# Performance work log

Hardware: AMD Instinct MI355X
Metric: run time of the kernel (lower is better)

The kernel has to match this reference:

```python
import jax, jax.numpy as jnp
import numpy as np

G_OFF = 1e-4
G_ON = 1e-3
K_V = 0.25
B, N_IN, N_OUT = 512, 512, 512


def setup_inputs() -> dict:
    key = jax.random.key(0)
    k1, k2 = jax.random.split(key)
    x = jax.random.normal(k1, (B, N_IN), dtype=jnp.float32)
    # build(): w ~ N(0, 1/sqrt(neurons_in)), b = zeros
    w = jax.random.normal(k2, (N_IN, N_OUT), dtype=jnp.float32) * (1.0 / np.sqrt(N_IN))
    b = jnp.zeros((N_OUT,), dtype=jnp.float32)
    return {"x": x, "w": w, "b": b}


def reference(x, w, b):
    # forward(): append ones column to inputs, bias row to weights
    inputs = jnp.concatenate([x, jnp.ones((x.shape[0], 1), dtype=x.dtype)], axis=1)  # [B, in+1]
    weights = jnp.concatenate([w, b[None, :]], axis=0)                               # [in+1, out]

    voltages = K_V * inputs

    # mapping.weights_to_conductances, rule='lowest':
    # differential pair per weight, interleaved (even=pos, odd=neg)
    max_weight = jnp.max(jnp.abs(weights))
    k_cond = (G_ON - G_OFF) / max_weight
    g_eff = k_cond * weights
    g_pos = G_OFF + jnp.maximum(g_eff, 0.0)
    g_neg = G_OFF + jnp.maximum(-g_eff, 0.0)
    conductances = jnp.stack([g_pos, g_neg], axis=-1).reshape(weights.shape[0], -1)  # [in+1, 2*out]

    # eval-mode branch: materialize per-element currents, then reduce over input axis
    individual_currents = voltages[:, :, None] * conductances[None, :, :]  # [B, in+1, 2*out]
    currents = jnp.sum(individual_currents, axis=1)                        # [B, 2*out]

    total_currents = currents[:, 0::2] - currents[:, 1::2]                 # [B, out]
    y_disturbed = total_currents / (K_V * k_cond)
    return y_disturbed
```

## Files before the change

### kernel.cpp

```cpp
#include <hip/hip_runtime.h>


constexpr int N_IN  = 512;
constexpr int N_OUT = 512;

__global__ __launch_bounds__(256) void memlin_gemm(
    const float* __restrict__ x,
    const float* __restrict__ w,
    const float* __restrict__ bias,
    float* __restrict__ y)
{
    const int t  = threadIdx.x;
    const int br = blockIdx.y;
    const int bc = blockIdx.x;

    const int lr  = t >> 3;
    const int lc4 = t & 7;

    __shared__ float xs[32][33];
    __shared__ float ws[32][32];

    float acc0 = 0.f, acc1 = 0.f, acc2 = 0.f, acc3 = 0.f;

    const float* xg = x + (br * 32 + lr) * N_IN + lc4 * 4;
    const float* wg = w + lr * N_OUT + bc * 32 + lc4 * 4;

    for (int k0 = 0; k0 < N_IN; k0 += 32) {
        const float4 xv = *reinterpret_cast<const float4*>(xg + k0);
        const float4 wv = *reinterpret_cast<const float4*>(wg + (size_t)k0 * N_OUT);

        xs[lr][lc4 * 4 + 0] = xv.x;
        xs[lr][lc4 * 4 + 1] = xv.y;
        xs[lr][lc4 * 4 + 2] = xv.z;
        xs[lr][lc4 * 4 + 3] = xv.w;
        *reinterpret_cast<float4*>(&ws[lr][lc4 * 4]) = wv;

        __syncthreads();

#pragma unroll
        for (int kk = 0; kk < 32; ++kk) {
            const float xa = xs[lr][kk];
            const float4 wr = *reinterpret_cast<const float4*>(&ws[kk][lc4 * 4]);
            acc0 = fmaf(xa, wr.x, acc0);
            acc1 = fmaf(xa, wr.y, acc1);
            acc2 = fmaf(xa, wr.z, acc2);
            acc3 = fmaf(xa, wr.w, acc3);
        }

        __syncthreads();
    }

    const float4 bv = *reinterpret_cast<const float4*>(bias + bc * 32 + lc4 * 4);
    float4 o;
    o.x = acc0 + bv.x;
    o.y = acc1 + bv.y;
    o.z = acc2 + bv.z;
    o.w = acc3 + bv.w;
    *reinterpret_cast<float4*>(y + (size_t)(br * 32 + lr) * N_OUT + bc * 32 + lc4 * 4) = o;
}

extern "C" void kernel_launch(void* const* d_in, const int* in_sizes, int n_in,
                              void* d_out, int out_size, void* d_ws, size_t ws_size,
                              hipStream_t stream) {
    const float* x  = (const float*)d_in[0];
    const float* w  = (const float*)d_in[1];
    const float* b  = (const float*)d_in[2];
    float* y        = (float*)d_out;

    dim3 grid(N_OUT / 32, 512 / 32);
    memlin_gemm<<<grid, 256, 0, stream>>>(x, w, b, y);
}
```

Measured before the change: 71.41 us.

## Convert inputs to bf16 and compute GEMM with MFMA 16x16x32 instructions

Adds a prep kernel that rounds x to bf16 and writes a transposed bf16 copy of w into workspace. The GEMM kernel then uses one wavefront per 32x32 tile, loading operands straight from global memory into registers and issuing bf16 MFMA instructions. This replaces the scalar FP32 FMA loop and its LDS staging with matrix-core throughput and half the operand bytes. The costs are an extra kernel launch, an uncoalesced strided read of w in the prep kernel, and lower precision from bf16 rounding of both operands.

```diff
diff --git a/kernel.cpp b/kernel.cpp
--- a/kernel.cpp
+++ b/kernel.cpp
@@ -1,62 +1,88 @@
 #include <hip/hip_runtime.h>
 
 
-constexpr int N_IN  = 512;
-constexpr int N_OUT = 512;
+constexpr int NB   = 512;
+constexpr int NK   = 512;
+constexpr int NN   = 512;
 
-__global__ __launch_bounds__(256) void memlin_gemm(
+using short8 = __attribute__((ext_vector_type(8))) short;
+using f32x4  = __attribute__((ext_vector_type(4))) float;
+
+__device__ inline unsigned short f2bf(float f) {
+    unsigned u = __builtin_bit_cast(unsigned, f);
+    u += 0x7FFFu + ((u >> 16) & 1u);
+    return (unsigned short)(u >> 16);
+}
+
+__global__ __launch_bounds__(256) void memlin_prep(
     const float* __restrict__ x,
     const float* __restrict__ w,
+    unsigned short* __restrict__ xb,
+    unsigned short* __restrict__ wt)
+{
+    const int t = blockIdx.x * 256 + threadIdx.x;
+
+    const float4 xv = reinterpret_cast<const float4*>(x)[t];
+    ushort4 xo;
+    xo.x = f2bf(xv.x); xo.y = f2bf(xv.y); xo.z = f2bf(xv.z); xo.w = f2bf(xv.w);
+    reinterpret_cast<ushort4*>(xb)[t] = xo;
+
+    const int c  = t >> 7;
+    const int k0 = (t & 127) * 4;
+    ushort4 wo;
+    wo.x = f2bf(w[(size_t)(k0 + 0) * NN + c]);
+    wo.y = f2bf(w[(size_t)(k0 + 1) * NN + c]);
+    wo.z = f2bf(w[(size_t)(k0 + 2) * NN + c]);
+    wo.w = f2bf(w[(size_t)(k0 + 3) * NN + c]);
+    reinterpret_cast<ushort4*>(wt)[t] = wo;
+}
+
+__global__ __launch_bounds__(64) void memlin_gemm(
+    const unsigned short* __restrict__ xb,
+    const unsigned short* __restrict__ wt,
     const float* __restrict__ bias,
     float* __restrict__ y)
 {
-    const int t  = threadIdx.x;
-    const int br = blockIdx.y;
-    const int bc = blockIdx.x;
+    const int l    = threadIdx.x;
+    const int row0 = blockIdx.y * 32;
+    const int col0 = blockIdx.x * 32;
+    const int lr   = l & 15;
+    const int kg   = l >> 4;
 
-    const int lr  = t >> 3;
-    const int lc4 = t & 7;
+    f32x4 acc00 = {0.f,0.f,0.f,0.f};
+    f32x4 acc01 = {0.f,0.f,0.f,0.f};
+    f32x4 acc10 = {0.f,0.f,0.f,0.f};
+    f32x4 acc11 = {0.f,0.f,0.f,0.f};
 
-    __shared__ float xs[32][33];
-    __shared__ float ws[32][32];
-
-    float acc0 = 0.f, acc1 = 0.f, acc2 = 0.f, acc3 = 0.f;
-
-    const float* xg = x + (br * 32 + lr) * N_IN + lc4 * 4;
-    const float* wg = w + lr * N_OUT + bc * 32 + lc4 * 4;
-
-    for (int k0 = 0; k0 < N_IN; k0 += 32) {
-        const float4 xv = *reinterpret_cast<const float4*>(xg + k0);
-        const float4 wv = *reinterpret_cast<const float4*>(wg + (size_t)k0 * N_OUT);
-
-        xs[lr][lc4 * 4 + 0] = xv.x;
-        xs[lr][lc4 * 4 + 1] = xv.y;
-        xs[lr][lc4 * 4 + 2] = xv.z;
-        xs[lr][lc4 * 4 + 3] = xv.w;
-        *reinterpret_cast<float4*>(&ws[lr][lc4 * 4]) = wv;
-
-        __syncthreads();
+    const unsigned short* xa0 = xb + (size_t)(row0 + lr) * NK + kg * 8;
+    const unsigned short* xa1 = xa0 + 16 * NK;
+    const unsigned short* wb0 = wt + (size_t)(col0 + lr) * NK + kg * 8;
+    const unsigned short* wb1 = wb0 + 16 * NK;
 
 #pragma unroll
-        for (int kk = 0; kk < 32; ++kk) {
-            const float xa = xs[lr][kk];
-            const float4 wr = *reinterpret_cast<const float4*>(&ws[kk][lc4 * 4]);
-            acc0 = fmaf(xa, wr.x, acc0);
-            acc1 = fmaf(xa, wr.y, acc1);
-            acc2 = fmaf(xa, wr.z, acc2);
-            acc3 = fmaf(xa, wr.w, acc3);
-        }
-
-        __syncthreads();
+    for (int k0 = 0; k0 < NK; k0 += 32) {
+        const short8 a0 = *reinterpret_cast<const short8*>(xa0 + k0);
+        const short8 a1 = *reinterpret_cast<const short8*>(xa1 + k0);
+        const short8 b0 = *reinterpret_cast<const short8*>(wb0 + k0);
+        const short8 b1 = *reinterpret_cast<const short8*>(wb1 + k0);
+        acc00 = __builtin_amdgcn_mfma_f32_16x16x32_bf16(a0, b0, acc00, 0, 0, 0);
+        acc01 = __builtin_amdgcn_mfma_f32_16x16x32_bf16(a0, b1, acc01, 0, 0, 0);
+        acc10 = __builtin_amdgcn_mfma_f32_16x16x32_bf16(a1, b0, acc10, 0, 0, 0);
+        acc11 = __builtin_amdgcn_mfma_f32_16x16x32_bf16(a1, b1, acc11, 0, 0, 0);
     }
 
-    const float4 bv = *reinterpret_cast<const float4*>(bias + bc * 32 + lc4 * 4);
-    float4 o;
-    o.x = acc0 + bv.x;
-    o.y = acc1 + bv.y;
-    o.z = acc2 + bv.z;
-    o.w = acc3 + bv.w;
-    *reinterpret_cast<float4*>(y + (size_t)(br * 32 + lr) * N_OUT + bc * 32 + lc4 * 4) = o;
+    const float bv0 = bias[col0 + lr];
+    const float bv1 = bias[col0 + 16 + lr];
+
+#pragma unroll
+    for (int r = 0; r < 4; ++r) {
+        const int rowA = row0 + kg * 4 + r;
+        const int rowB = rowA + 16;
+        y[(size_t)rowA * NN + col0 + lr]      = acc00[r] + bv0;
+        y[(size_t)rowA * NN + col0 + 16 + lr] = acc01[r] + bv1;
+        y[(size_t)rowB * NN + col0 + lr]      = acc10[r] + bv0;
+        y[(size_t)rowB * NN + col0 + 16 + lr] = acc11[r] + bv1;
+    }
 }
 
 extern "C" void kernel_launch(void* const* d_in, const int* in_sizes, int n_in,
@@ -67,6 +93,11 @@
     const float* b  = (const float*)d_in[2];
     float* y        = (float*)d_out;
 
-    dim3 grid(N_OUT / 32, 512 / 32);
-    memlin_gemm<<<grid, 256, 0, stream>>>(x, w, b, y);
+    unsigned short* xb = (unsigned short*)d_ws;
+    unsigned short* wt = xb + (size_t)NB * NK;
+
+    memlin_prep<<<dim3(256), dim3(256), 0, stream>>>(x, w, xb, wt);
+
+    dim3 grid(NN / 32, NB / 32);
+    memlin_gemm<<<grid, dim3(64), 0, stream>>>(xb, wt, b, y);
 }
```

New measurement: 64.11 us. 10.2% less time.

## Replace FP32 LDS-tiled GEMM with bf16 MFMA single-wave tiles

Applied to the files above, without the earlier changes.

Swaps the shared-memory FP32 FMA GEMM for a kernel in which each 64-thread wave computes a 16x16 output tile using the 16x16x32 bf16 MFMA instruction. Operands are loaded straight from global memory and rounded to bf16 in registers, with no LDS staging or barriers. The grid grows to 1024 small blocks. This trades accuracy (bf16 inputs) for matrix-core throughput, and the uncoalesced strided loads of w columns and the lack of any operand reuse could limit the benefit.

```diff
diff --git a/kernel.cpp b/kernel.cpp
--- a/kernel.cpp
+++ b/kernel.cpp
@@ -1,62 +1,65 @@
 #include <hip/hip_runtime.h>
 
 
-constexpr int N_IN  = 512;
-constexpr int N_OUT = 512;
+constexpr int NK = 512;
+constexpr int NN = 512;
 
-__global__ __launch_bounds__(256) void memlin_gemm(
+using short8 = __attribute__((ext_vector_type(8))) short;
+using f32x4  = __attribute__((ext_vector_type(4))) float;
+
+__device__ inline unsigned pack_bf16x2(float f0, float f1) {
+    unsigned u0 = __builtin_bit_cast(unsigned, f0) + 0x8000u;
+    unsigned u1 = __builtin_bit_cast(unsigned, f1) + 0x8000u;
+    return __builtin_amdgcn_perm(u1, u0, 0x07060302u);
+}
+
+__global__ __launch_bounds__(64, 1) void memlin_fused(
     const float* __restrict__ x,
     const float* __restrict__ w,
     const float* __restrict__ bias,
     float* __restrict__ y)
 {
-    const int t  = threadIdx.x;
-    const int br = blockIdx.y;
-    const int bc = blockIdx.x;
+    const int l    = threadIdx.x;
+    const int row0 = blockIdx.y * 16;
+    const int col0 = blockIdx.x * 16;
+    const int lr   = l & 15;
+    const int kg   = l >> 4;
 
-    const int lr  = t >> 3;
-    const int lc4 = t & 7;
+    f32x4 acc = {0.f, 0.f, 0.f, 0.f};
 
-    __shared__ float xs[32][33];
-    __shared__ float ws[32][32];
-
-    float acc0 = 0.f, acc1 = 0.f, acc2 = 0.f, acc3 = 0.f;
-
-    const float* xg = x + (br * 32 + lr) * N_IN + lc4 * 4;
-    const float* wg = w + lr * N_OUT + bc * 32 + lc4 * 4;
-
-    for (int k0 = 0; k0 < N_IN; k0 += 32) {
-        const float4 xv = *reinterpret_cast<const float4*>(xg + k0);
-        const float4 wv = *reinterpret_cast<const float4*>(wg + (size_t)k0 * N_OUT);
-
-        xs[lr][lc4 * 4 + 0] = xv.x;
-        xs[lr][lc4 * 4 + 1] = xv.y;
-        xs[lr][lc4 * 4 + 2] = xv.z;
-        xs[lr][lc4 * 4 + 3] = xv.w;
-        *reinterpret_cast<float4*>(&ws[lr][lc4 * 4]) = wv;
-
-        __syncthreads();
+    const float* xrow = x + (size_t)(row0 + lr) * NK + kg * 8;
+    const float* wcol = w + (size_t)(kg * 8) * NN + (col0 + lr);
 
 #pragma unroll
-        for (int kk = 0; kk < 32; ++kk) {
-            const float xa = xs[lr][kk];
-            const float4 wr = *reinterpret_cast<const float4*>(&ws[kk][lc4 * 4]);
-            acc0 = fmaf(xa, wr.x, acc0);
-            acc1 = fmaf(xa, wr.y, acc1);
-            acc2 = fmaf(xa, wr.z, acc2);
-            acc3 = fmaf(xa, wr.w, acc3);
-        }
+    for (int step = 0; step < 16; ++step) {
+        const int k0 = step * 32;
 
-        __syncthreads();
+        const float4 a0 = *reinterpret_cast<const float4*>(xrow + k0);
+        const float4 a1 = *reinterpret_cast<const float4*>(xrow + k0 + 4);
+
+        const float* wp = wcol + (size_t)k0 * NN;
+        float b0 = wp[0 * NN], b1 = wp[1 * NN], b2 = wp[2 * NN], b3 = wp[3 * NN];
+        float b4 = wp[4 * NN], b5 = wp[5 * NN], b6 = wp[6 * NN], b7 = wp[7 * NN];
+
+        union { unsigned u[4]; short8 s; } fa, fb;
+        fa.u[0] = pack_bf16x2(a0.x, a0.y);
+        fa.u[1] = pack_bf16x2(a0.z, a0.w);
+        fa.u[2] = pack_bf16x2(a1.x, a1.y);
+        fa.u[3] = pack_bf16x2(a1.z, a1.w);
+        fb.u[0] = pack_bf16x2(b0, b1);
+        fb.u[1] = pack_bf16x2(b2, b3);
+        fb.u[2] = pack_bf16x2(b4, b5);
+        fb.u[3] = pack_bf16x2(b6, b7);
+
+        acc = __builtin_amdgcn_mfma_f32_16x16x32_bf16(fa.s, fb.s, acc, 0, 0, 0);
     }
 
-    const float4 bv = *reinterpret_cast<const float4*>(bias + bc * 32 + lc4 * 4);
-    float4 o;
-    o.x = acc0 + bv.x;
-    o.y = acc1 + bv.y;
-    o.z = acc2 + bv.z;
-    o.w = acc3 + bv.w;
-    *reinterpret_cast<float4*>(y + (size_t)(br * 32 + lr) * N_OUT + bc * 32 + lc4 * 4) = o;
+    const float bv = bias[col0 + lr];
+#pragma unroll
+    for (int r = 0; r < 4; ++r) {
+        const int row = row0 + kg * 4 + r;
+        y[(size_t)row * NN + col0 + lr] = acc[r] + bv;
+    }
 }
 
 extern "C" void kernel_launch(void* const* d_in, const int* in_sizes, int n_in,
@@ -67,6 +70,6 @@
     const float* b  = (const float*)d_in[2];
     float* y        = (float*)d_out;
 
-    dim3 grid(N_OUT / 32, 512 / 32);
-    memlin_gemm<<<grid, 256, 0, stream>>>(x, w, b, y);
+    dim3 grid(NN / 16, 512 / 16);
+    memlin_fused<<<grid, dim3(64), 0, stream>>>(x, w, b, y);
 }
```

New measurement: 61.56 us. 13.8% less time.
